# Performance work log

Hardware: AMD Instinct MI355X
Metric: run time of the kernel (lower is better)

The kernel has to match this reference:

```python
import jax, jax.numpy as jnp
import numpy as np

EPS = 1e-5

def _layernorm(h, g, b):
    mu = jnp.mean(h, axis=-1, keepdims=True)
    var = jnp.mean(jnp.square(h - mu), axis=-1, keepdims=True)
    return (h - mu) * jax.lax.rsqrt(var + EPS) * g + b

def setup_inputs() -> dict:
    key = jax.random.key(0)
    ks = jax.random.split(key, 16)
    N, E, H = 100000, 500000, 128
    x = jax.random.normal(ks[0], (N, H), dtype=jnp.float32)
    edge_index = jax.random.randint(ks[1], (2, E), 0, N, dtype=jnp.int64)
    edge = jax.random.normal(ks[2], (E, H), dtype=jnp.float32)
    def lin(k, fan_in, fan_out):
        bound = 1.0 / np.sqrt(fan_in)
        k1, k2 = jax.random.split(k)
        W = jax.random.uniform(k1, (fan_in, fan_out), jnp.float32, -bound, bound)
        b = jax.random.uniform(k2, (fan_out,), jnp.float32, -bound, bound)
        return W, b
    W0, b0 = lin(ks[3], 3 * H, H)
    W1, b1 = lin(ks[4], H, H)
    W2, b2 = lin(ks[5], H, H)
    W3, b3 = lin(ks[6], H, 1)
    g0 = jnp.ones((H,), jnp.float32); be0 = jnp.zeros((H,), jnp.float32)
    g1 = jnp.ones((H,), jnp.float32); be1 = jnp.zeros((H,), jnp.float32)
    g2 = jnp.ones((H,), jnp.float32); be2 = jnp.zeros((H,), jnp.float32)
    return dict(x=x, edge_index=edge_index, edge=edge,
                W0=W0, b0=b0, g0=g0, be0=be0,
                W1=W1, b1=b1, g1=g1, be1=be1,
                W2=W2, b2=b2, g2=g2, be2=be2,
                W3=W3, b3=b3)

def reference(x, edge_index, edge, W0, b0, g0, be0, W1, b1, g1, be1, W2, b2, g2, be2, W3, b3):
    src, dst = edge_index[0], edge_index[1]
    # gather + concat: [E, 3*H]
    h = jnp.concatenate([x[src], x[dst], edge], axis=-1)
    h = jax.nn.relu(_layernorm(h @ W0 + b0, g0, be0))
    h = jax.nn.relu(_layernorm(h @ W1 + b1, g1, be1))
    h = jax.nn.relu(_layernorm(h @ W2 + b2, g2, be2))
    out = h @ W3 + b3  # [E, 1]
    return jnp.squeeze(out, axis=-1)
```

## Files before the change

kernel.cpp:

```cpp
#include <hip/hip_runtime.h>

typedef _Float16 f16;
typedef _Float16 f16x8 __attribute__((ext_vector_type(8)));
typedef _Float16 f16x4 __attribute__((ext_vector_type(4)));
typedef float    f32x4 __attribute__((ext_vector_type(4)));

static constexpr int H   = 128;
static constexpr int MT  = 128;
static constexpr int WCH = 4096;
static constexpr int NCH = 20;
static constexpr size_t WS_NEED = (size_t)NCH * WCH * sizeof(f16);

__global__ __launch_bounds__(256)
void wprep(const float* __restrict__ W0, const float* __restrict__ W1,
           const float* __restrict__ W2, f16* __restrict__ ws)
{
    int e = blockIdx.x * 256 + threadIdx.x;
    if (e >= NCH * WCH) return;
    int cid = e >> 12;
    int rem = e & 4095;
    int k   = rem >> 7;
    int n   = rem & 127;
    const float* W; int k0;
    if (cid < 12)      { W = W0; k0 = cid * 32; }
    else if (cid < 16) { W = W1; k0 = (cid - 12) * 32; }
    else               { W = W2; k0 = (cid - 16) * 32; }
    f16 v = (f16)W[(size_t)(k0 + k) * H + n];
    int su = (k >> 3) ^ ((n >> 2) & 3);
    ws[cid * WCH + n * 32 + su * 8 + (k & 7)] = v;
}

__device__ __forceinline__ void glds16(const f16* g, f16* l) {
    __builtin_amdgcn_global_load_lds((const __attribute__((address_space(1))) void*)g,
                                     (__attribute__((address_space(3))) void*)l, 16, 0, 0);
}

template <int WPRE>
__global__ __launch_bounds__(256, 3)
void edge_mlp_fused(const float* __restrict__ x,
                    const int* __restrict__ eidx,
                    const float* __restrict__ edge,
                    const f16* __restrict__ wpre,
                    const float* __restrict__ W0, const float* __restrict__ b0,
                    const float* __restrict__ g0, const float* __restrict__ be0,
                    const float* __restrict__ W1, const float* __restrict__ b1,
                    const float* __restrict__ g1, const float* __restrict__ be1,
                    const float* __restrict__ W2, const float* __restrict__ b2,
                    const float* __restrict__ g2, const float* __restrict__ be2,
                    const float* __restrict__ W3, const float* __restrict__ b3,
                    float* __restrict__ out, int E)
{
    __shared__ __align__(16) f16 wch[2 * WCH];
    __shared__ __align__(16) f16 uni[MT * H];

    const int tid  = threadIdx.x;
    const int lane = tid & 63;
    const int wid  = tid >> 6;
    const int c    = lane & 15;
    const int g    = lane >> 4;
    const int wrow = wid * 32;
    const long long e0 = (long long)blockIdx.x * MT;

    const int r_ = lane >> 1;
    const int hf = lane & 1;
    long long er = e0 + wrow + r_; if (er >= E) er = (long long)E - 1;
    const float* psrc = x    + (size_t)eidx[er]     * H;
    const float* pdst = x    + (size_t)eidx[E + er] * H;
    const float* pedg = edge + (size_t)er           * H;

    f16* aslice = &uni[wid * 1024];
    const int s_    = (r_ >> 2) & 3;
    const int aoff0 = r_ * 32 + ((2 * hf)     ^ s_) * 8;
    const int aoff1 = r_ * 32 + ((2 * hf + 1) ^ s_) * 8;
    const int sw    = (g ^ ((c >> 2) & 3)) * 8;

    f32x4 acc[8][2];
    #pragma unroll
    for (int t = 0; t < 8; ++t) {
        acc[t][0] = f32x4{0.f, 0.f, 0.f, 0.f};
        acc[t][1] = f32x4{0.f, 0.f, 0.f, 0.f};
    }

    float4 apf0, apf1, apf2, apf3;
    auto issueA = [&](int kc) {
        const float* bptr = (kc < 4) ? psrc : (kc < 8) ? pdst : pedg;
        const float4* p = (const float4*)(bptr + (kc & 3) * 32 + hf * 16);
        apf0 = p[0]; apf1 = p[1]; apf2 = p[2]; apf3 = p[3];
    };
    auto writeA = [&]() {
        f16x8 lo, hi;
        lo[0] = (f16)apf0.x; lo[1] = (f16)apf0.y; lo[2] = (f16)apf0.z; lo[3] = (f16)apf0.w;
        lo[4] = (f16)apf1.x; lo[5] = (f16)apf1.y; lo[6] = (f16)apf1.z; lo[7] = (f16)apf1.w;
        hi[0] = (f16)apf2.x; hi[1] = (f16)apf2.y; hi[2] = (f16)apf2.z; hi[3] = (f16)apf2.w;
        hi[4] = (f16)apf3.x; hi[5] = (f16)apf3.y; hi[6] = (f16)apf3.z; hi[7] = (f16)apf3.w;
        *(f16x8*)&aslice[aoff0] = lo;
        *(f16x8*)&aslice[aoff1] = hi;
    };

    auto stageW = [&](int cid, int pbuf) {
        f16* dst = &wch[pbuf * WCH];
        if (WPRE) {
            const f16* src = wpre + (size_t)cid * WCH + wid * 1024;
            f16* d = dst + wid * 1024;
            glds16(src + (lane << 3), d);
            glds16(src + 512 + (lane << 3), d + 512);
        } else {
            const float* W = (cid < 12) ? W0 : (cid < 16) ? W1 : W2;
            int k0 = ((cid < 12) ? cid : (cid < 16) ? (cid - 12) : (cid - 16)) * 32;
            #pragma unroll
            for (int i = 0; i < 4; ++i) {
                int f  = i * 256 + tid;
                int n  = f & 127;
                int kq = f >> 7;
                const float* pw = W + (size_t)(k0 + kq * 4) * H + n;
                f16x4 v;
                v[0] = (f16)pw[0]; v[1] = (f16)pw[H]; v[2] = (f16)pw[2 * H]; v[3] = (f16)pw[3 * H];
                int su = (kq >> 1) ^ ((n >> 2) & 3);
                *(f16x4*)&dst[n * 32 + su * 8 + (kq & 1) * 4] = v;
            }
        }
    };

    auto mfma_ach = [&](int pbuf) {
        const f16* wb = &wch[pbuf * WCH];
        f16x8 a0 = *(const f16x8*)&aslice[c * 32 + sw];
        f16x8 a1 = *(const f16x8*)&aslice[(16 + c) * 32 + sw];
        #pragma unroll
        for (int t = 0; t < 8; ++t) {
            f16x8 bf = *(const f16x8*)&wb[(t * 16 + c) * 32 + sw];
            acc[t][0] = __builtin_amdgcn_mfma_f32_16x16x32_f16(a0, bf, acc[t][0], 0, 0, 0);
            acc[t][1] = __builtin_amdgcn_mfma_f32_16x16x32_f16(a1, bf, acc[t][1], 0, 0, 0);
        }
    };
    auto mfma_act = [&](int koff, int pbuf) {
        const f16* wb = &wch[pbuf * WCH];
        int col = (koff + g * 8) ^ ((c & 7) << 3);
        f16x8 a0 = *(const f16x8*)&uni[(wrow + c) * H + col];
        f16x8 a1 = *(const f16x8*)&uni[(wrow + 16 + c) * H + col];
        #pragma unroll
        for (int t = 0; t < 8; ++t) {
            f16x8 bf = *(const f16x8*)&wb[(t * 16 + c) * 32 + sw];
            acc[t][0] = __builtin_amdgcn_mfma_f32_16x16x32_f16(a0, bf, acc[t][0], 0, 0, 0);
            acc[t][1] = __builtin_amdgcn_mfma_f32_16x16x32_f16(a1, bf, acc[t][1], 0, 0, 0);
        }
    };

    auto ln_relu_store = [&](const float* __restrict__ bias,
                             const float* __restrict__ gamma,
                             const float* __restrict__ beta) {
        float mu[2][4], rs[2][4];
        #pragma unroll
        for (int t = 0; t < 8; ++t) {
            float bt = bias[t * 16 + c];
            #pragma unroll
            for (int s = 0; s < 2; ++s)
                #pragma unroll
                for (int r = 0; r < 4; ++r) acc[t][s][r] += bt;
        }
        #pragma unroll
        for (int s = 0; s < 2; ++s)
            #pragma unroll
            for (int r = 0; r < 4; ++r) {
                float v = 0.f, q = 0.f;
                #pragma unroll
                for (int t = 0; t < 8; ++t) { float a = acc[t][s][r]; v += a; q += a * a; }
                #pragma unroll
                for (int m = 1; m < 16; m <<= 1) {
                    v += __shfl_xor(v, m, 64);
                    q += __shfl_xor(q, m, 64);
                }
                float mean = v * (1.0f / H);
                float var  = q * (1.0f / H) - mean * mean;
                mu[s][r] = mean;
                rs[s][r] = rsqrtf(var + 1e-5f);
            }
        #pragma unroll
        for (int t = 0; t < 8; ++t) {
            float gm = gamma[t * 16 + c];
            float bb = beta[t * 16 + c];
            #pragma unroll
            for (int s = 0; s < 2; ++s)
                #pragma unroll
                for (int r = 0; r < 4; ++r) {
                    float v = (acc[t][s][r] - mu[s][r]) * rs[s][r] * gm + bb;
                    v = fmaxf(v, 0.f);
                    int row = wrow + s * 16 + g * 4 + r;
                    uni[row * H + ((t * 16 + c) ^ ((row & 7) << 3))] = (f16)v;
                }
        }
        #pragma unroll
        for (int t = 0; t < 8; ++t) {
            acc[t][0] = f32x4{0.f, 0.f, 0.f, 0.f};
            acc[t][1] = f32x4{0.f, 0.f, 0.f, 0.f};
        }
    };

    stageW(0, 0);
    issueA(0);
    __syncthreads();

    #pragma unroll 2
    for (int kc = 0; kc < 12; ++kc) {
        stageW(kc + 1, (kc + 1) & 1);
        writeA();
        if (kc < 11) issueA(kc + 1);
        mfma_ach(kc & 1);
        __syncthreads();
    }
    ln_relu_store(b0, g0, be0);

    #pragma unroll 2
    for (int kc = 0; kc < 4; ++kc) {
        stageW(13 + kc, (kc + 1) & 1);
        mfma_act(kc * 32, kc & 1);
        __syncthreads();
    }
    ln_relu_store(b1, g1, be1);

    #pragma unroll 2
    for (int kc = 0; kc < 4; ++kc) {
        if (kc < 3) stageW(17 + kc, (kc + 1) & 1);
        mfma_act(kc * 32, kc & 1);
        if (kc < 3) __syncthreads();
    }

    {
        float mu[2][4], rs[2][4];
        #pragma unroll
        for (int t = 0; t < 8; ++t) {
            float bt = b2[t * 16 + c];
            #pragma unroll
            for (int s = 0; s < 2; ++s)
                #pragma unroll
                for (int r = 0; r < 4; ++r) acc[t][s][r] += bt;
        }
        #pragma unroll
        for (int s = 0; s < 2; ++s)
            #pragma unroll
            for (int r = 0; r < 4; ++r) {
                float v = 0.f, q = 0.f;
                #pragma unroll
                for (int t = 0; t < 8; ++t) { float a = acc[t][s][r]; v += a; q += a * a; }
                #pragma unroll
                for (int m = 1; m < 16; m <<= 1) {
                    v += __shfl_xor(v, m, 64);
                    q += __shfl_xor(q, m, 64);
                }
                float mean = v * (1.0f / H);
                float var  = q * (1.0f / H) - mean * mean;
                mu[s][r] = mean;
                rs[s][r] = rsqrtf(var + 1e-5f);
            }
        float po[2][4] = {{0.f,0.f,0.f,0.f},{0.f,0.f,0.f,0.f}};
        #pragma unroll
        for (int t = 0; t < 8; ++t) {
            float gm  = g2[t * 16 + c];
            float bb  = be2[t * 16 + c];
            float w3v = W3[t * 16 + c];
            #pragma unroll
            for (int s = 0; s < 2; ++s)
                #pragma unroll
                for (int r = 0; r < 4; ++r) {
                    float v = (acc[t][s][r] - mu[s][r]) * rs[s][r] * gm + bb;
                    v = fmaxf(v, 0.f);
                    po[s][r] += v * w3v;
                }
        }
        #pragma unroll
        for (int s = 0; s < 2; ++s)
            #pragma unroll
            for (int r = 0; r < 4; ++r) {
                #pragma unroll
                for (int m = 1; m < 16; m <<= 1) po[s][r] += __shfl_xor(po[s][r], m, 64);
            }
        if (c == 0) {
            float bb3 = b3[0];
            #pragma unroll
            for (int s = 0; s < 2; ++s) {
                long long eb = e0 + wrow + s * 16 + g * 4;
                if (eb + 3 < E) {
                    float4 o;
                    o.x = po[s][0] + bb3; o.y = po[s][1] + bb3;
                    o.z = po[s][2] + bb3; o.w = po[s][3] + bb3;
                    *(float4*)(out + eb) = o;
                } else {
                    #pragma unroll
                    for (int r = 0; r < 4; ++r)
                        if (eb + r < E) out[eb + r] = po[s][r] + bb3;
                }
            }
        }
    }
}

extern "C" void kernel_launch(void* const* d_in, const int* in_sizes, int n_in,
                              void* d_out, int out_size, void* d_ws, size_t ws_size,
                              hipStream_t stream)
{
    const float* x    = (const float*)d_in[0];
    const int*   eidx = (const int*)d_in[1];
    const float* edge = (const float*)d_in[2];
    const float* W0   = (const float*)d_in[3];
    const float* b0   = (const float*)d_in[4];
    const float* g0   = (const float*)d_in[5];
    const float* be0  = (const float*)d_in[6];
    const float* W1   = (const float*)d_in[7];
    const float* b1   = (const float*)d_in[8];
    const float* g1   = (const float*)d_in[9];
    const float* be1  = (const float*)d_in[10];
    const float* W2   = (const float*)d_in[11];
    const float* b2   = (const float*)d_in[12];
    const float* g2   = (const float*)d_in[13];
    const float* be2  = (const float*)d_in[14];
    const float* W3   = (const float*)d_in[15];
    const float* b3   = (const float*)d_in[16];
    float*       out  = (float*)d_out;

    const int E = in_sizes[1] / 2;
    const int grid = (E + MT - 1) / MT;

    if (d_ws && ws_size >= WS_NEED) {
        f16* wsp = (f16*)d_ws;
        hipLaunchKernelGGL(wprep, dim3((NCH * WCH + 255) / 256), dim3(256), 0, stream,
                           W0, W1, W2, wsp);
        hipLaunchKernelGGL((edge_mlp_fused<1>), dim3(grid), dim3(256), 0, stream,
                           x, eidx, edge, (const f16*)wsp,
                           W0, b0, g0, be0, W1, b1, g1, be1, W2, b2, g2, be2,
                           W3, b3, out, E);
    } else {
        hipLaunchKernelGGL((edge_mlp_fused<0>), dim3(grid), dim3(256), 0, stream,
                           x, eidx, edge, (const f16*)nullptr,
                           W0, b0, g0, be0, W1, b1, g1, be1, W2, b2, g2, be2,
                           W3, b3, out, E);
    }
}
```

Measured before the change: 603.7 us.

## Load layer-0 gathered inputs directly into MFMA operand registers, skipping LDS staging

Each lane now loads its own MFMA A-operand fragment (rows c and 16+c, 8 consecutive features) straight from the gathered x/edge rows and converts it to f16 in registers. This removes the per-chunk LDS write and read of the A tile in layer 0. The activation swizzle widens from row&7 to row&15, and launch bounds drop from 3 to 2 blocks per CU to give more registers for the prefetch. In exchange, each lane issues narrower 32-byte global loads for two rows, and occupancy may fall.

```diff
diff --git a/kernel.cpp b/kernel.cpp
--- a/kernel.cpp
+++ b/kernel.cpp
@@ -36,7 +36,7 @@
 }
 
 template <int WPRE>
-__global__ __launch_bounds__(256, 3)
+__global__ __launch_bounds__(256, 2)
 void edge_mlp_fused(const float* __restrict__ x,
                     const int* __restrict__ eidx,
                     const float* __restrict__ edge,
@@ -51,7 +51,7 @@
                     float* __restrict__ out, int E)
 {
     __shared__ __align__(16) f16 wch[2 * WCH];
-    __shared__ __align__(16) f16 uni[MT * H];
+    __shared__ __align__(16) f16 act[MT * H];
 
     const int tid  = threadIdx.x;
     const int lane = tid & 63;
@@ -61,18 +61,14 @@
     const int wrow = wid * 32;
     const long long e0 = (long long)blockIdx.x * MT;
 
-    const int r_ = lane >> 1;
-    const int hf = lane & 1;
-    long long er = e0 + wrow + r_; if (er >= E) er = (long long)E - 1;
-    const float* psrc = x    + (size_t)eidx[er]     * H;
-    const float* pdst = x    + (size_t)eidx[E + er] * H;
-    const float* pedg = edge + (size_t)er           * H;
-
-    f16* aslice = &uni[wid * 1024];
-    const int s_    = (r_ >> 2) & 3;
-    const int aoff0 = r_ * 32 + ((2 * hf)     ^ s_) * 8;
-    const int aoff1 = r_ * 32 + ((2 * hf + 1) ^ s_) * 8;
-    const int sw    = (g ^ ((c >> 2) & 3)) * 8;
+    long long er0 = e0 + wrow + c;      if (er0 >= E) er0 = (long long)E - 1;
+    long long er1 = e0 + wrow + 16 + c; if (er1 >= E) er1 = (long long)E - 1;
+    const float* ps0 = x    + (size_t)eidx[er0]     * H;
+    const float* ps1 = x    + (size_t)eidx[er1]     * H;
+    const float* pd0 = x    + (size_t)eidx[E + er0] * H;
+    const float* pd1 = x    + (size_t)eidx[E + er1] * H;
+    const float* pe0 = edge + (size_t)er0           * H;
+    const float* pe1 = edge + (size_t)er1           * H;
 
     f32x4 acc[8][2];
     #pragma unroll
@@ -83,18 +79,16 @@
 
     float4 apf0, apf1, apf2, apf3;
     auto issueA = [&](int kc) {
-        const float* bptr = (kc < 4) ? psrc : (kc < 8) ? pdst : pedg;
-        const float4* p = (const float4*)(bptr + (kc & 3) * 32 + hf * 16);
-        apf0 = p[0]; apf1 = p[1]; apf2 = p[2]; apf3 = p[3];
-    };
-    auto writeA = [&]() {
-        f16x8 lo, hi;
-        lo[0] = (f16)apf0.x; lo[1] = (f16)apf0.y; lo[2] = (f16)apf0.z; lo[3] = (f16)apf0.w;
-        lo[4] = (f16)apf1.x; lo[5] = (f16)apf1.y; lo[6] = (f16)apf1.z; lo[7] = (f16)apf1.w;
-        hi[0] = (f16)apf2.x; hi[1] = (f16)apf2.y; hi[2] = (f16)apf2.z; hi[3] = (f16)apf2.w;
-        hi[4] = (f16)apf3.x; hi[5] = (f16)apf3.y; hi[6] = (f16)apf3.z; hi[7] = (f16)apf3.w;
-        *(f16x8*)&aslice[aoff0] = lo;
-        *(f16x8*)&aslice[aoff1] = hi;
+        const float* q0 = ((kc < 4) ? ps0 : (kc < 8) ? pd0 : pe0) + (kc & 3) * 32 + g * 8;
+        const float* q1 = ((kc < 4) ? ps1 : (kc < 8) ? pd1 : pe1) + (kc & 3) * 32 + g * 8;
+        apf0 = ((const float4*)q0)[0]; apf1 = ((const float4*)q0)[1];
+        apf2 = ((const float4*)q1)[0]; apf3 = ((const float4*)q1)[1];
+    };
+    auto cvtA = [&](f16x8& a0, f16x8& a1) {
+        a0[0] = (f16)apf0.x; a0[1] = (f16)apf0.y; a0[2] = (f16)apf0.z; a0[3] = (f16)apf0.w;
+        a0[4] = (f16)apf1.x; a0[5] = (f16)apf1.y; a0[6] = (f16)apf1.z; a0[7] = (f16)apf1.w;
+        a1[0] = (f16)apf2.x; a1[1] = (f16)apf2.y; a1[2] = (f16)apf2.z; a1[3] = (f16)apf2.w;
+        a1[4] = (f16)apf3.x; a1[5] = (f16)apf3.y; a1[6] = (f16)apf3.z; a1[7] = (f16)apf3.w;
     };
 
     auto stageW = [&](int cid, int pbuf) {
@@ -121,10 +115,10 @@
         }
     };
 
-    auto mfma_ach = [&](int pbuf) {
+    const int sw = (g ^ ((c >> 2) & 3)) * 8;
+
+    auto mfma_reg = [&](f16x8 a0, f16x8 a1, int pbuf) {
         const f16* wb = &wch[pbuf * WCH];
-        f16x8 a0 = *(const f16x8*)&aslice[c * 32 + sw];
-        f16x8 a1 = *(const f16x8*)&aslice[(16 + c) * 32 + sw];
         #pragma unroll
         for (int t = 0; t < 8; ++t) {
             f16x8 bf = *(const f16x8*)&wb[(t * 16 + c) * 32 + sw];
@@ -134,9 +128,9 @@
     };
     auto mfma_act = [&](int koff, int pbuf) {
         const f16* wb = &wch[pbuf * WCH];
-        int col = (koff + g * 8) ^ ((c & 7) << 3);
-        f16x8 a0 = *(const f16x8*)&uni[(wrow + c) * H + col];
-        f16x8 a1 = *(const f16x8*)&uni[(wrow + 16 + c) * H + col];
+        int col = (koff + g * 8) ^ (c << 3);
+        f16x8 a0 = *(const f16x8*)&act[(wrow + c) * H + col];
+        f16x8 a1 = *(const f16x8*)&act[(wrow + 16 + c) * H + col];
         #pragma unroll
         for (int t = 0; t < 8; ++t) {
             f16x8 bf = *(const f16x8*)&wb[(t * 16 + c) * 32 + sw];
@@ -185,7 +179,7 @@
                     float v = (acc[t][s][r] - mu[s][r]) * rs[s][r] * gm + bb;
                     v = fmaxf(v, 0.f);
                     int row = wrow + s * 16 + g * 4 + r;
-                    uni[row * H + ((t * 16 + c) ^ ((row & 7) << 3))] = (f16)v;
+                    act[row * H + ((t * 16 + c) ^ ((row & 15) << 3))] = (f16)v;
                 }
         }
         #pragma unroll
@@ -201,10 +195,11 @@
 
     #pragma unroll 2
     for (int kc = 0; kc < 12; ++kc) {
+        f16x8 a0, a1;
+        cvtA(a0, a1);
+        if (kc < 11) issueA(kc + 1);
         stageW(kc + 1, (kc + 1) & 1);
-        writeA();
-        if (kc < 11) issueA(kc + 1);
-        mfma_ach(kc & 1);
+        mfma_reg(a0, a1, kc & 1);
         __syncthreads();
     }
     ln_relu_store(b0, g0, be0);
```

Measured after the change: 819.3 us. 1.36x slower.
